# Kernel tuning notes

Measured on AMD Instinct MI355X. Metric: run time of the kernel, lower is better.

## Reference

```python
import jax, jax.numpy as jnp
import numpy as np

B, C, T, F = 2, 256, 1024, 64
N, HID = 4, 64


def setup_inputs() -> dict:
    key = jax.random.key(0)
    ks = jax.random.split(key, 9)
    s = 0.02
    return {
        "x": jax.random.normal(ks[0], (B, C, T, F), dtype=jnp.float32),
        "Wq": jax.random.normal(ks[1], (N, HID, C), dtype=jnp.float32) * s,
        "bq": jnp.zeros((N, HID), dtype=jnp.float32),
        "Wk": jax.random.normal(ks[2], (N, HID, C), dtype=jnp.float32) * s,
        "bk": jnp.zeros((N, HID), dtype=jnp.float32),
        "Wv": jax.random.normal(ks[3], (N, C // N, C), dtype=jnp.float32) * s,
        "bv": jnp.zeros((N, C // N), dtype=jnp.float32),
        "Wp": jax.random.normal(ks[4], (C, C), dtype=jnp.float32) * s,
        "bp": jnp.zeros((C,), dtype=jnp.float32),
    }


def reference(x, Wq, bq, Wk, bk, Wv, bv, Wp, bp):
    b, c, t, f = x.shape
    n = Wq.shape[0]
    # conv1x1 per head then torch: cat(dim=0) -> [N*b, h, t, f]; transpose(1,2); flatten -> [N*b, t, h*f]
    def proj(W, bias):
        h = W.shape[1]
        y = jnp.einsum('bctf,nhc->nbthf', x, W) + bias[:, None, None, :, None]
        return y.reshape(n * b, t, h * f)

    Q = proj(Wq, bq)                       # [N*b, t, hid*f]
    K = proj(Wk, bk)                       # [N*b, t, hid*f]
    V = proj(Wv, bv)                       # [N*b, t, (c/N)*f]

    scale = 1.0 / jnp.sqrt(jnp.asarray(Q.shape[-1], dtype=x.dtype))
    attn = jax.nn.softmax(jnp.einsum('mte,mse->mts', Q, K) * scale, axis=2)
    Vo = jnp.einsum('mts,msd->mtd', attn, V)             # [N*b, t, c*f/N]

    # torch: reshape(b*N, t, c*f//N).transpose(1,2).view(N,b,c//N,t,f).transpose(0,1).view(b,c,t,f)
    Vo = Vo.transpose(0, 2, 1)                            # [N*b, c*f/N, t]
    Vo = Vo.reshape(n, b, c // n, t, f)
    Vo = jnp.swapaxes(Vo, 0, 1).reshape(b, c, t, f)

    out = jnp.einsum('bctf,oc->botf', Vo, Wp) + bp[None, :, None, None]
    return out + x
```

## Files before the change

### kernel.cpp

```cpp
#include <hip/hip_runtime.h>

#define DI __device__ __forceinline__

static constexpr int B_ = 2;
static constexpr int C_ = 256;
static constexpr int T_ = 1024;
static constexpr int F_ = 64;
static constexpr int M_ = 8;
static constexpr int E_ = 4096;
static constexpr float SCALE_ = 1.0f / 64.0f;

typedef __attribute__((ext_vector_type(8))) short bf16x8;
typedef __attribute__((ext_vector_type(4))) float f32x4;

DI unsigned short bf16_rne(float f) {
    unsigned int u = __float_as_uint(f);
    return (unsigned short)((u + 0x7FFFu + ((u >> 16) & 1u)) >> 16);
}
DI float bf2f(unsigned short h) { return __uint_as_float(((unsigned int)h) << 16); }
DI ushort4 pack4(float a, float b, float c, float d) {
    return make_ushort4(bf16_rne(a), bf16_rne(b), bf16_rne(c), bf16_rne(d));
}
DI float4 up4(ushort4 u) {
    return make_float4(bf2f(u.x), bf2f(u.y), bf2f(u.z), bf2f(u.w));
}

DI void gload_lds16(const unsigned short* g, unsigned short* l) {
    __builtin_amdgcn_global_load_lds(
        (const __attribute__((address_space(1))) unsigned int*)g,
        (__attribute__((address_space(3))) unsigned int*)l, 16, 0, 0);
}

DI void mfma16(f32x4& acc, bf16x8 a, bf16x8 b) {
    asm("v_mfma_f32_16x16x32_bf16 %0, %1, %2, %0" : "+v"(acc) : "v"(a), "v"(b));
}

__global__ __launch_bounds__(256) void wconv_kernel(
    const float* __restrict__ Wq, const float* __restrict__ Wk,
    const float* __restrict__ Wv, const float* __restrict__ Wp,
    const float* __restrict__ bq, const float* __restrict__ bk,
    const float* __restrict__ bv,
    unsigned short* __restrict__ Wall, unsigned short* __restrict__ Wpb,
    float* __restrict__ bias_all)
{
    const int tid = (int)threadIdx.x;
    const int bid = (int)blockIdx.x;
    if (bid < 192) {
        const int idx = (bid * 256 + tid) * 4;
        const int proj = idx >> 16, rem = idx & 65535;
        const float* src = proj == 0 ? Wq : (proj == 1 ? Wk : Wv);
        float4 v = *(const float4*)(src + rem);
        *(ushort4*)(Wall + idx) = pack4(v.x, v.y, v.z, v.w);
        const int gid = bid * 256 + tid;
        if (gid < 768) {
            float bb = gid < 256 ? bq[gid] : (gid < 512 ? bk[gid - 256] : bv[gid - 512]);
            bias_all[gid] = bb;
        }
    } else {
        const int idx = ((bid - 192) * 256 + tid) * 4;
        float4 v = *(const float4*)(Wp + idx);
        *(ushort4*)(Wpb + idx) = pack4(v.x, v.y, v.z, v.w);
    }
}

__global__ __launch_bounds__(256) void qkv_one(
    const float* __restrict__ x, const unsigned short* __restrict__ Wall,
    const float* __restrict__ bias_all, unsigned short* __restrict__ outQ)
{
    const int wgid = (int)blockIdx.x;
    const int b = wgid >> 9, tft = wgid & 511;
    const int tfbase = tft * 128;

    const int tid = (int)threadIdx.x;
    const int wid = tid >> 6, lane = tid & 63;
    const int wr = wid >> 1, wc = wid & 1;
    const int lo16 = lane & 15, hi4 = lane >> 4;

    __shared__ unsigned short As[4 * 128 * 64];
    __shared__ unsigned short Bs[128 * 64];

    {
        const int a = lane & 7, cg = lane >> 3;
        const int rowb = wid * 32 + a * 4;
        const float* xb = x + (size_t)b * (C_ * T_ * F_) + tfbase + rowb;
        for (int cb = 0; cb < 256; cb += 64) {
            const int c0 = cb + cg * 8;
            float4 v[8];
#pragma unroll
            for (int g = 0; g < 8; ++g)
                v[g] = *(const float4*)(xb + (size_t)(c0 + g) * 65536);
            const int kc = cb >> 6;
#pragma unroll
            for (int j = 0; j < 4; ++j) {
                const int row = rowb + j;
                const int col8 = cg ^ (row & 7);
                float e0 = (&v[0].x)[j], e1 = (&v[1].x)[j], e2 = (&v[2].x)[j], e3 = (&v[3].x)[j];
                float e4 = (&v[4].x)[j], e5 = (&v[5].x)[j], e6 = (&v[6].x)[j], e7 = (&v[7].x)[j];
                ushort4 p0 = pack4(e0, e1, e2, e3);
                ushort4 p1 = pack4(e4, e5, e6, e7);
                *(ushort4*)&As[kc * 8192 + row * 64 + col8 * 8]     = p0;
                *(ushort4*)&As[kc * 8192 + row * 64 + col8 * 8 + 4] = p1;
            }
        }
    }

    const int srow = lane >> 3;
    const int scol = ((lane & 7) ^ srow) * 8;
    const int tf0 = tfbase + wr * 64;

    __syncthreads();

    for (int ntl = 0; ntl < 6; ++ntl) {
        const int nbase = ntl * 128;
        const unsigned short* brow = Wall + (size_t)nbase * 256;
        f32x4 acc[4][4] = {};

        for (int kc = 0; kc < 4; ++kc) {
#pragma unroll
            for (int i = 0; i < 4; ++i) {
                const int rb = wid * 32 + i * 8;
                gload_lds16(brow + (size_t)(rb + srow) * 256 + kc * 64 + scol,
                            &Bs[rb * 64]);
            }
            __syncthreads();
#pragma unroll
            for (int kk = 0; kk < 2; ++kk) {
                const int hc = (kk * 32 + hi4 * 8) ^ ((lane & 7) << 3);
                bf16x8 a[4], bb[4];
#pragma unroll
                for (int mi = 0; mi < 4; ++mi)
                    a[mi] = *(const bf16x8*)&As[kc * 8192 + (wr * 64 + mi * 16 + lo16) * 64 + hc];
#pragma unroll
                for (int nj = 0; nj < 4; ++nj)
                    bb[nj] = *(const bf16x8*)&Bs[(wc * 64 + nj * 16 + lo16) * 64 + hc];
#pragma unroll
                for (int mi = 0; mi < 4; ++mi)
#pragma unroll
                    for (int nj = 0; nj < 4; ++nj)
                        mfma16(acc[mi][nj], a[mi], bb[nj]);
            }
            __syncthreads();
        }

        asm volatile("s_nop 7\n\ts_nop 7" ::: "memory");
#pragma unroll
        for (int nj = 0; nj < 4; ++nj) {
            const int r_col = nbase + wc * 64 + nj * 16 + lo16;
            const int projl = r_col >> 8;
            const int rr = r_col & 255;
            const int mrow = (rr >> 6) * 2 + b;
            const int h = rr & 63;
            const float bv = bias_all[r_col];
            unsigned short* dst0 = outQ + (size_t)projl * 33554432
                                 + (size_t)mrow * (T_ * E_) + h * 64;
#pragma unroll
            for (int mi = 0; mi < 4; ++mi) {
                const int tf = tf0 + mi * 16 + hi4 * 4;
                const int t = tf >> 6, f = tf & 63;
                *(ushort4*)(dst0 + (size_t)t * E_ + f) =
                    pack4(acc[mi][nj][0] + bv, acc[mi][nj][1] + bv,
                          acc[mi][nj][2] + bv, acc[mi][nj][3] + bv);
            }
        }
        if (ntl < 5) __syncthreads();
    }
}

__global__ __launch_bounds__(256) void scores_mfma(
    const unsigned short* __restrict__ Q, const unsigned short* __restrict__ K,
    unsigned short* __restrict__ S)
{
    const int orig = (int)blockIdx.x;
    const int wg = (orig & 7) * 64 + (orig >> 3);
    const int m = wg >> 6;
    const int rest = wg & 63;
    const int sbase = (rest & 7) * 128;
    const int tbase = (rest >> 3) * 128;
    const int tid = (int)threadIdx.x;
    const int wid = tid >> 6, lane = tid & 63;
    const int wr = wid >> 1, wc = wid & 1;
    const int lo16 = lane & 15, hi4 = lane >> 4;

    __shared__ unsigned short As[128 * 64];
    __shared__ unsigned short Bs[128 * 64];

    f32x4 acc[4][4] = {};

    const unsigned short* qrow = Q + ((size_t)m * T_ + tbase) * E_;
    const unsigned short* krow = K + ((size_t)m * T_ + sbase) * E_;

    const int srow = lane >> 3;
    const int scol = ((lane & 7) ^ srow) * 8;

    for (int eb = 0; eb < E_; eb += 64) {
#pragma unroll
        for (int i = 0; i < 4; ++i) {
            const int rb = wid * 32 + i * 8;
            gload_lds16(qrow + (size_t)(rb + srow) * E_ + eb + scol, &As[rb * 64]);
            gload_lds16(krow + (size_t)(rb + srow) * E_ + eb + scol, &Bs[rb * 64]);
        }
        __syncthreads();
#pragma unroll
        for (int kk = 0; kk < 2; ++kk) {
            const int hc = (kk * 32 + hi4 * 8) ^ ((lane & 7) << 3);
            bf16x8 a[4], bb[4];
#pragma unroll
            for (int mi = 0; mi < 4; ++mi)
                a[mi] = *(const bf16x8*)&As[(wr * 64 + mi * 16 + lo16) * 64 + hc];
#pragma unroll
            for (int nj = 0; nj < 4; ++nj)
                bb[nj] = *(const bf16x8*)&Bs[(wc * 64 + nj * 16 + lo16) * 64 + hc];
#pragma unroll
            for (int mi = 0; mi < 4; ++mi)
#pragma unroll
                for (int nj = 0; nj < 4; ++nj)
                    mfma16(acc[mi][nj], a[mi], bb[nj]);
        }
        __syncthreads();
    }

    asm volatile("s_nop 7\n\ts_nop 7" ::: "memory");
#pragma unroll
    for (int mi = 0; mi < 4; ++mi)
#pragma unroll
        for (int r = 0; r < 4; ++r) {
            int trow = tbase + wr * 64 + mi * 16 + hi4 * 4 + r;
            unsigned short* sp = S + ((size_t)m * T_ + trow) * T_ + sbase + wc * 64 + lo16;
#pragma unroll
            for (int nj = 0; nj < 4; ++nj)
                sp[nj * 16] = bf16_rne(acc[mi][nj][r] * SCALE_);
        }
}

__global__ __launch_bounds__(256) void softmax_kernel(
    const unsigned short* __restrict__ S, unsigned short* __restrict__ A)
{
    const int tid = (int)threadIdx.x;
    const int wid = tid >> 6, lane = tid & 63;
    const size_t rowoff = ((size_t)blockIdx.x * 4 + wid) * 1024;

    const size_t off = rowoff + lane * 16;
    bf16x8 u0 = *(const bf16x8*)(S + off);
    bf16x8 u1 = *(const bf16x8*)(S + off + 8);

    float v[16];
#pragma unroll
    for (int i = 0; i < 8; ++i) {
        v[i]     = bf2f((unsigned short)u0[i]);
        v[i + 8] = bf2f((unsigned short)u1[i]);
    }

    float mx = v[0];
#pragma unroll
    for (int i = 1; i < 16; ++i) mx = fmaxf(mx, v[i]);
#pragma unroll
    for (int off2 = 32; off2 > 0; off2 >>= 1) mx = fmaxf(mx, __shfl_xor(mx, off2));

    float sm = 0.f;
#pragma unroll
    for (int i = 0; i < 16; ++i) { v[i] = __expf(v[i] - mx); sm += v[i]; }
#pragma unroll
    for (int off2 = 32; off2 > 0; off2 >>= 1) sm += __shfl_xor(sm, off2);
    const float inv = 1.0f / sm;

    bf16x8 r0, r1;
#pragma unroll
    for (int i = 0; i < 8; ++i) {
        r0[i] = (short)bf16_rne(v[i] * inv);
        r1[i] = (short)bf16_rne(v[i + 8] * inv);
    }
    *(bf16x8*)(A + off)     = r0;
    *(bf16x8*)(A + off + 8) = r1;
}

__global__ __launch_bounds__(256) void vt_kernel(
    const unsigned short* __restrict__ V, unsigned short* __restrict__ Vt)
{
    const int m = blockIdx.z;
    const int d0 = blockIdx.x * 64;
    const int s0 = blockIdx.y * 64;
    const int tid = (int)threadIdx.x;
    __shared__ unsigned short ts[64][68];

    const unsigned short* vp = V + (size_t)m * T_ * E_;
#pragma unroll
    for (int it = 0; it < 4; ++it) {
        int idx = it * 256 + tid;
        int sl = idx >> 4, d4 = (idx & 15) * 4;
        *(ushort4*)&ts[sl][d4] = *(const ushort4*)&vp[(size_t)(s0 + sl) * E_ + d0 + d4];
    }
    __syncthreads();
    unsigned short* op = Vt + (size_t)m * E_ * T_;
    const int dl = tid >> 2, s16 = (tid & 3) * 16;
#pragma unroll
    for (int q = 0; q < 4; ++q) {
        int s4 = s16 + q * 4;
        ushort4 v = make_ushort4(ts[s4][dl], ts[s4+1][dl], ts[s4+2][dl], ts[s4+3][dl]);
        *(ushort4*)&op[(size_t)(d0 + dl) * T_ + s0 + s4] = v;
    }
}

__global__ __launch_bounds__(256) void pv_mfma(
    const unsigned short* __restrict__ A, const unsigned short* __restrict__ Vt,
    unsigned short* __restrict__ G)
{
    const int orig = (int)blockIdx.x;
    const int wg = (orig & 7) * 256 + (orig >> 3);
    const int m = wg >> 8;
    const int rest = wg & 255;
    const int dbase = (rest & 31) * 128;
    const int tbase = (rest >> 5) * 128;
    const int nh = m >> 1, b = m & 1;
    const int tid = (int)threadIdx.x;
    const int wid = tid >> 6, lane = tid & 63;
    const int wr = wid >> 1, wc = wid & 1;
    const int lo16 = lane & 15, hi4 = lane >> 4;

    __shared__ unsigned short As[128 * 64];
    __shared__ unsigned short Bs[128 * 64];

    f32x4 acc[4][4] = {};

    const unsigned short* arow = A  + ((size_t)m * T_ + tbase) * T_;
    const unsigned short* vrow = Vt + (size_t)m * E_ * T_ + (size_t)dbase * T_;

    const int srow = lane >> 3;
    const int scol = ((lane & 7) ^ srow) * 8;

    for (int sb = 0; sb < T_; sb += 64) {
#pragma unroll
        for (int i = 0; i < 4; ++i) {
            const int rb = wid * 32 + i * 8;
            gload_lds16(arow + (size_t)(rb + srow) * T_ + sb + scol, &As[rb * 64]);
            gload_lds16(vrow + (size_t)(rb + srow) * T_ + sb + scol, &Bs[rb * 64]);
        }
        __syncthreads();
#pragma unroll
        for (int kk = 0; kk < 2; ++kk) {
            const int hc = (kk * 32 + hi4 * 8) ^ ((lane & 7) << 3);
            bf16x8 a[4], bb[4];
#pragma unroll
            for (int mi = 0; mi < 4; ++mi)
                a[mi] = *(const bf16x8*)&As[(wr * 64 + mi * 16 + lo16) * 64 + hc];
#pragma unroll
            for (int nj = 0; nj < 4; ++nj)
                bb[nj] = *(const bf16x8*)&Bs[(wc * 64 + nj * 16 + lo16) * 64 + hc];
#pragma unroll
            for (int mi = 0; mi < 4; ++mi)
#pragma unroll
                for (int nj = 0; nj < 4; ++nj)
                    mfma16(acc[mi][nj], a[mi], bb[nj]);
        }
        __syncthreads();
    }

    asm volatile("s_nop 7\n\ts_nop 7" ::: "memory");
    const int cb   = nh * 64 + (dbase >> 6) + wc;
    const int t2lo = (tbase >> 6) + wr;
#pragma unroll
    for (int mi = 0; mi < 4; ++mi) {
        const int tl = mi * 16 + hi4 * 4;
#pragma unroll
        for (int nj = 0; nj < 4; ++nj) {
            const int d63 = nj * 16 + lo16;
            size_t addr = (((size_t)(b * 256 + cb)) * 1024 + d63 * 16 + t2lo) * 64 + tl;
            *(ushort4*)&G[addr] = pack4(acc[mi][nj][0], acc[mi][nj][1],
                                        acc[mi][nj][2], acc[mi][nj][3]);
        }
    }
}

__global__ __launch_bounds__(256) void gt_kernel(
    const unsigned short* __restrict__ G, unsigned short* __restrict__ GT)
{
    const int tf0 = blockIdx.x * 64;
    const int c0  = blockIdx.y * 64;
    const int b   = blockIdx.z;
    const int tid = (int)threadIdx.x;
    __shared__ unsigned short ts[64][68];

    const unsigned short* gb = G + (size_t)(b * 256 + c0) * 65536 + tf0;
#pragma unroll
    for (int it = 0; it < 4; ++it) {
        int idx = it * 256 + tid;
        int cl = idx >> 4, tf4 = (idx & 15) * 4;
        *(ushort4*)&ts[cl][tf4] = *(const ushort4*)(gb + (size_t)cl * 65536 + tf4);
    }
    __syncthreads();
    const int tfl = tid >> 2, c16 = (tid & 3) * 16;
    unsigned short* op = GT + ((size_t)b * 65536 + tf0 + tfl) * 256 + c0 + c16;
#pragma unroll
    for (int q = 0; q < 4; ++q) {
        int cl = c16 + q * 4;
        ushort4 v = make_ushort4(ts[cl][tfl], ts[cl+1][tfl], ts[cl+2][tfl], ts[cl+3][tfl]);
        *(ushort4*)(op + q * 4) = v;
    }
}

__global__ __launch_bounds__(256) void outproj_mfma(
    const unsigned short* __restrict__ GT, const unsigned short* __restrict__ Wpb,
    const float* __restrict__ bp, const float* __restrict__ x,
    float* __restrict__ out)
{
    const int tfbase = blockIdx.x * 128;
    const int obase  = blockIdx.y * 128;
    const int b      = blockIdx.z;
    const int tid = (int)threadIdx.x;
    const int wid = tid >> 6, lane = tid & 63;
    const int wr = wid >> 1, wc = wid & 1;
    const int lo16 = lane & 15, hi4 = lane >> 4;

    __shared__ unsigned short As[128 * 64];
    __shared__ unsigned short Bs[128 * 64];

    f32x4 acc[4][4] = {};

    const unsigned short* arow = GT + ((size_t)b * 65536 + tfbase) * 256;
    const unsigned short* brow = Wpb + (size_t)obase * 256;

    const int srow = lane >> 3;
    const int scol = ((lane & 7) ^ srow) * 8;

    for (int cb = 0; cb < 256; cb += 64) {
#pragma unroll
        for (int i = 0; i < 4; ++i) {
            const int rb = wid * 32 + i * 8;
            gload_lds16(arow + (size_t)(rb + srow) * 256 + cb + scol, &As[rb * 64]);
            gload_lds16(brow + (size_t)(rb + srow) * 256 + cb + scol, &Bs[rb * 64]);
        }
        __syncthreads();
#pragma unroll
        for (int kk = 0; kk < 2; ++kk) {
            const int hc = (kk * 32 + hi4 * 8) ^ ((lane & 7) << 3);
            bf16x8 a[4], bb[4];
#pragma unroll
            for (int mi = 0; mi < 4; ++mi)
                a[mi] = *(const bf16x8*)&As[(wr * 64 + mi * 16 + lo16) * 64 + hc];
#pragma unroll
            for (int nj = 0; nj < 4; ++nj)
                bb[nj] = *(const bf16x8*)&Bs[(wc * 64 + nj * 16 + lo16) * 64 + hc];
#pragma unroll
            for (int mi = 0; mi < 4; ++mi)
#pragma unroll
                for (int nj = 0; nj < 4; ++nj)
                    mfma16(acc[mi][nj], a[mi], bb[nj]);
        }
        __syncthreads();
    }

    asm volatile("s_nop 7\n\ts_nop 7" ::: "memory");
#pragma unroll
    for (int nj = 0; nj < 4; ++nj) {
        const int o = obase + wc * 64 + nj * 16 + lo16;
        const float bias = bp[o];
        const size_t rowb = ((size_t)(b * 256 + o)) * 65536;
#pragma unroll
        for (int mi = 0; mi < 4; ++mi) {
            const int tf = tfbase + wr * 64 + mi * 16 + hi4 * 4;
            float4 xv = *(const float4*)(x + rowb + tf);
            float4 r = make_float4(acc[mi][nj][0] + bias + xv.x,
                                   acc[mi][nj][1] + bias + xv.y,
                                   acc[mi][nj][2] + bias + xv.z,
                                   acc[mi][nj][3] + bias + xv.w);
            *(float4*)(out + rowb + tf) = r;
        }
    }
}

extern "C" void kernel_launch(void* const* d_in, const int* in_sizes, int n_in,
                              void* d_out, int out_size, void* d_ws, size_t ws_size,
                              hipStream_t stream) {
    const float* x  = (const float*)d_in[0];
    const float* Wq = (const float*)d_in[1];
    const float* bq = (const float*)d_in[2];
    const float* Wk = (const float*)d_in[3];
    const float* bk = (const float*)d_in[4];
    const float* Wv = (const float*)d_in[5];
    const float* bv = (const float*)d_in[6];
    const float* Wp = (const float*)d_in[7];
    const float* bp = (const float*)d_in[8];
    float* out = (float*)d_out;

    char* ws = (char*)d_ws;
    unsigned short* Q    = (unsigned short*)(ws);
    unsigned short* K    = (unsigned short*)(ws + 67108864);
    unsigned short* V    = (unsigned short*)(ws + 134217728);
    unsigned short* S    = (unsigned short*)(ws + 201326592);
    unsigned short* A    = (unsigned short*)(ws + 218103808);
    unsigned short* Wall = (unsigned short*)(ws + 234881024);
    float* bias_all      = (float*)(ws + 235274240);
    unsigned short* Wpb  = (unsigned short*)(ws + 235277312);
    unsigned short* Vt = K;
    unsigned short* G  = Q;
    unsigned short* GT = V;

    wconv_kernel<<<256, 256, 0, stream>>>(Wq, Wk, Wv, Wp, bq, bk, bv, Wall, Wpb, bias_all);
    qkv_one<<<1024, 256, 0, stream>>>(x, Wall, bias_all, Q);
    scores_mfma<<<512, 256, 0, stream>>>(Q, K, S);
    softmax_kernel<<<2048, 256, 0, stream>>>(S, A);
    vt_kernel<<<dim3(64, 16, M_), 256, 0, stream>>>(V, Vt);
    pv_mfma<<<2048, 256, 0, stream>>>(A, Vt, G);
    gt_kernel<<<dim3(1024, 4, 2), 256, 0, stream>>>(G, GT);
    outproj_mfma<<<dim3(512, 2, 2), 256, 0, stream>>>(GT, Wpb, bp, x, out);
}
```

Baseline: 408.3 us.

## Fuse G transpose into output projection and stagger QKV tile order

Removes the separate gt_kernel by having the output-projection kernel read G in its native channel-major layout and transpose it into swizzled shared memory while staging the A tile. This drops one full write and read of the G intermediate in HBM and one kernel launch. It also rotates the N-tile and K-chunk iteration order per workgroup in the QKV projection, so that concurrent blocks touch different weight rows and L2 contention drops. The in-register transpose adds scalar LDS stores per thread, which could cost some of the outproj efficiency.

```diff
diff --git a/kernel.cpp b/kernel.cpp
--- a/kernel.cpp
+++ b/kernel.cpp
@@ -108,14 +108,19 @@
     const int scol = ((lane & 7) ^ srow) * 8;
     const int tf0 = tfbase + wr * 64;
 
+    const int krot = wgid & 3;
+    int nrot = wgid % 6;
+
     __syncthreads();
 
-    for (int ntl = 0; ntl < 6; ++ntl) {
+    for (int ntl_i = 0; ntl_i < 6; ++ntl_i) {
+        int ntl = ntl_i + nrot; if (ntl >= 6) ntl -= 6;
         const int nbase = ntl * 128;
         const unsigned short* brow = Wall + (size_t)nbase * 256;
         f32x4 acc[4][4] = {};
 
-        for (int kc = 0; kc < 4; ++kc) {
+        for (int kc_i = 0; kc_i < 4; ++kc_i) {
+            const int kc = (kc_i + krot) & 3;
 #pragma unroll
             for (int i = 0; i < 4; ++i) {
                 const int rb = wid * 32 + i * 8;
@@ -162,7 +167,7 @@
                           acc[mi][nj][2] + bv, acc[mi][nj][3] + bv);
             }
         }
-        if (ntl < 5) __syncthreads();
+        if (ntl_i < 5) __syncthreads();
     }
 }
 
@@ -370,35 +375,8 @@
     }
 }
 
-__global__ __launch_bounds__(256) void gt_kernel(
-    const unsigned short* __restrict__ G, unsigned short* __restrict__ GT)
-{
-    const int tf0 = blockIdx.x * 64;
-    const int c0  = blockIdx.y * 64;
-    const int b   = blockIdx.z;
-    const int tid = (int)threadIdx.x;
-    __shared__ unsigned short ts[64][68];
-
-    const unsigned short* gb = G + (size_t)(b * 256 + c0) * 65536 + tf0;
-#pragma unroll
-    for (int it = 0; it < 4; ++it) {
-        int idx = it * 256 + tid;
-        int cl = idx >> 4, tf4 = (idx & 15) * 4;
-        *(ushort4*)&ts[cl][tf4] = *(const ushort4*)(gb + (size_t)cl * 65536 + tf4);
-    }
-    __syncthreads();
-    const int tfl = tid >> 2, c16 = (tid & 3) * 16;
-    unsigned short* op = GT + ((size_t)b * 65536 + tf0 + tfl) * 256 + c0 + c16;
-#pragma unroll
-    for (int q = 0; q < 4; ++q) {
-        int cl = c16 + q * 4;
-        ushort4 v = make_ushort4(ts[cl][tfl], ts[cl+1][tfl], ts[cl+2][tfl], ts[cl+3][tfl]);
-        *(ushort4*)(op + q * 4) = v;
-    }
-}
-
-__global__ __launch_bounds__(256) void outproj_mfma(
-    const unsigned short* __restrict__ GT, const unsigned short* __restrict__ Wpb,
+__global__ __launch_bounds__(256) void outproj_fused(
+    const unsigned short* __restrict__ G, const unsigned short* __restrict__ Wpb,
     const float* __restrict__ bp, const float* __restrict__ x,
     float* __restrict__ out)
 {
@@ -415,18 +393,35 @@
 
     f32x4 acc[4][4] = {};
 
-    const unsigned short* arow = GT + ((size_t)b * 65536 + tfbase) * 256;
     const unsigned short* brow = Wpb + (size_t)obase * 256;
 
     const int srow = lane >> 3;
     const int scol = ((lane & 7) ^ srow) * 8;
 
+    const int cg = tid >> 4;
+    const int ag = tid & 15;
+
     for (int cb = 0; cb < 256; cb += 64) {
 #pragma unroll
         for (int i = 0; i < 4; ++i) {
             const int rb = wid * 32 + i * 8;
-            gload_lds16(arow + (size_t)(rb + srow) * 256 + cb + scol, &As[rb * 64]);
             gload_lds16(brow + (size_t)(rb + srow) * 256 + cb + scol, &Bs[rb * 64]);
+        }
+        {
+            const unsigned short* gb = G + ((size_t)(b * 256 + cb + cg * 4)) * 65536
+                                     + tfbase + ag * 8;
+            bf16x8 vv0 = *(const bf16x8*)(gb);
+            bf16x8 vv1 = *(const bf16x8*)(gb + 65536);
+            bf16x8 vv2 = *(const bf16x8*)(gb + 2 * 65536);
+            bf16x8 vv3 = *(const bf16x8*)(gb + 3 * 65536);
+#pragma unroll
+            for (int j = 0; j < 8; ++j) {
+                const int row = ag * 8 + j;
+                const int phys = row * 64 + ((((cg >> 1) ^ (row & 7)) << 3) + (cg & 1) * 4);
+                ushort4 w = make_ushort4((unsigned short)vv0[j], (unsigned short)vv1[j],
+                                         (unsigned short)vv2[j], (unsigned short)vv3[j]);
+                *(ushort4*)&As[phys] = w;
+            }
         }
         __syncthreads();
 #pragma unroll
@@ -492,7 +487,6 @@
     unsigned short* Wpb  = (unsigned short*)(ws + 235277312);
     unsigned short* Vt = K;
     unsigned short* G  = Q;
-    unsigned short* GT = V;
 
     wconv_kernel<<<256, 256, 0, stream>>>(Wq, Wk, Wv, Wp, bq, bk, bv, Wall, Wpb, bias_all);
     qkv_one<<<1024, 256, 0, stream>>>(x, Wall, bias_all, Q);
@@ -500,6 +494,5 @@
     softmax_kernel<<<2048, 256, 0, stream>>>(S, A);
     vt_kernel<<<dim3(64, 16, M_), 256, 0, stream>>>(V, Vt);
     pv_mfma<<<2048, 256, 0, stream>>>(A, Vt, G);
-    gt_kernel<<<dim3(1024, 4, 2), 256, 0, stream>>>(G, GT);
-    outproj_mfma<<<dim3(512, 2, 2), 256, 0, stream>>>(GT, Wpb, bp, x, out);
-}
+    outproj_fused<<<dim3(512, 2, 2), 256, 0, stream>>>(G, Wpb, bp, x, out);
+}
```

Result: faster. 396.3 us (median of 3 runs) (-2.9%).
